# Optimization experiments

Measured on AMD Instinct MI355X. Metric: run time of the kernel, lower is better.

Reference implementation:

```python
import jax, jax.numpy as jnp
import numpy as np

NUM_GROUPS = 8
EPS = 1e-5


def setup_inputs() -> dict:
    key = jax.random.key(0)
    ks = jax.random.split(key, 4)
    C = 128
    x = jax.random.normal(ks[0], (4, C, 64, 64), dtype=jnp.float32)
    gn_weight = jnp.ones((C,), dtype=jnp.float32)
    gn_bias = jnp.zeros((C,), dtype=jnp.float32)
    qkv_weight = jax.random.normal(ks[1], (3 * C, C), dtype=jnp.float32) * (C ** -0.5)
    qkv_bias = jnp.zeros((3 * C,), dtype=jnp.float32)
    proj_weight = jax.random.normal(ks[2], (C, C), dtype=jnp.float32) * (C ** -0.5)
    proj_bias = jnp.zeros((C,), dtype=jnp.float32)
    return {
        "x": x,
        "gn_weight": gn_weight,
        "gn_bias": gn_bias,
        "qkv_weight": qkv_weight,
        "qkv_bias": qkv_bias,
        "proj_weight": proj_weight,
        "proj_bias": proj_bias,
    }


def reference(x, gn_weight, gn_bias, qkv_weight, qkv_bias, proj_weight, proj_bias):
    b, c, h, w = x.shape
    scale = c ** (-0.5)

    # GroupNorm(8, c): normalize over (channels_in_group, h, w)
    xg = x.reshape(b, NUM_GROUPS, c // NUM_GROUPS, h, w)
    mean = jnp.mean(xg, axis=(2, 3, 4), keepdims=True)
    var = jnp.var(xg, axis=(2, 3, 4), keepdims=True)
    xn = ((xg - mean) * jax.lax.rsqrt(var + EPS)).reshape(b, c, h, w)
    xn = xn * gn_weight[None, :, None, None] + gn_bias[None, :, None, None]

    # 1x1 conv QKV == channel matmul; flatten spatial to sequence n = h*w
    xn_flat = xn.reshape(b, c, h * w)  # [b, c, n]
    qkv = jnp.einsum('oc,bcn->bno', qkv_weight, xn_flat) + qkv_bias  # [b, n, 3c]
    q, k, v = qkv[..., :c], qkv[..., c:2 * c], qkv[..., 2 * c:]

    # attention: materializes [b, n, n] scores as in original
    attn = jnp.einsum('bnc,bmc->bnm', q, k) * scale
    attn = jax.nn.softmax(attn, axis=-1)
    out = jnp.einsum('bnm,bmc->bnc', attn, v)  # [b, n, c]

    # proj 1x1 conv + residual
    out = jnp.einsum('oc,bnc->bno', proj_weight, out) + proj_bias  # [b, n, c]
    out = out.transpose(0, 2, 1).reshape(b, c, h, w)
    return x + out
```

## Files before the change

### kernel.cpp

```cpp
#include <hip/hip_runtime.h>

#define BATCH 4
#define CCH 128
#define NSP 4096
#define NGRP 8
#define GROUP_ELEMS 65536
#define QSCALE 0.12751744f
#define EPS_GN 1e-5f
#define KHN 4
#define OPSTRIDE 2097152
#define LPSTRIDE 16384

typedef short s8b __attribute__((ext_vector_type(8)));
typedef float f32x4 __attribute__((ext_vector_type(4)));
typedef float f32x16 __attribute__((ext_vector_type(16)));

static __device__ __forceinline__ short f2bf(float f) {
  union { float f; unsigned u; } v; v.f = f;
  unsigned r = (v.u + 0x7FFFu + ((v.u >> 16) & 1u)) >> 16;
  return (short)r;
}

static __device__ __forceinline__ float bf2f(short s) {
  unsigned u = ((unsigned)(unsigned short)s) << 16;
  float f; __builtin_memcpy(&f, &u, 4); return f;
}

static __device__ __forceinline__ float fexp2(float x) {
#if __has_builtin(__builtin_amdgcn_exp2f)
  return __builtin_amdgcn_exp2f(x);
#else
  return exp2f(x);
#endif
}

static __device__ __forceinline__ unsigned cvtpk(float a, float b) {
  unsigned r;
  asm("v_cvt_pk_bf16_f32 %0, %1, %2" : "=v"(r) : "v"(a), "v"(b));
  return r;
}

static __device__ __forceinline__ s8b pack8(float a0, float a1, float a2, float a3,
                                            float a4, float a5, float a6, float a7) {
  union { unsigned u[4]; s8b v; } x;
  x.u[0] = cvtpk(a0, a1); x.u[1] = cvtpk(a2, a3);
  x.u[2] = cvtpk(a4, a5); x.u[3] = cvtpk(a6, a7);
  return x.v;
}

static __device__ __forceinline__ f32x4 mfma16(s8b a, s8b b, f32x4 c) {
  return __builtin_amdgcn_mfma_f32_16x16x32_bf16(a, b, c, 0, 0, 0);
}
static __device__ __forceinline__ f32x16 mfma32(s8b a, s8b b, f32x16 c) {
  return __builtin_amdgcn_mfma_f32_32x32x16_bf16(a, b, c, 0, 0, 0);
}

static __device__ __forceinline__ void async16(const void* g, void* l) {
  __builtin_amdgcn_global_load_lds(
      (const __attribute__((address_space(1))) void*)g,
      (__attribute__((address_space(3))) void*)l, 16, 0, 0);
}

__global__ void gn_stats(const float* __restrict__ x, float* __restrict__ part) {
  int bx = blockIdx.x;
  int ch = bx & 7, bg = bx >> 3;
  const float* base = x + (size_t)bg * GROUP_ELEMS + (size_t)ch * 8192;
  int t = threadIdx.x;
  float s = 0.f, ss = 0.f;
  #pragma unroll
  for (int i = 0; i < 8; ++i) {
    float4 v = *(const float4*)(base + i * 1024 + t * 4);
    s  += v.x + v.y + v.z + v.w;
    ss += v.x * v.x + v.y * v.y + v.z * v.z + v.w * v.w;
  }
  #pragma unroll
  for (int off = 1; off < 64; off <<= 1) {
    s  += __shfl_xor(s, off);
    ss += __shfl_xor(ss, off);
  }
  __shared__ float red[8];
  int w = t >> 6;
  if ((t & 63) == 0) { red[w * 2] = s; red[w * 2 + 1] = ss; }
  __syncthreads();
  if (t == 0) {
    part[bx * 2]     = red[0] + red[2] + red[4] + red[6];
    part[bx * 2 + 1] = red[1] + red[3] + red[5] + red[7];
  }
}

__global__ void gn_apply(const float* __restrict__ x, const float* __restrict__ gw,
                         const float* __restrict__ gb, const float* __restrict__ part,
                         short* __restrict__ xn) {
  int bx = blockIdx.x;
  int ns = bx & 7, g = (bx >> 3) & 7, b = bx >> 6;
  int bg = b * NGRP + g;
  float s = 0.f, ss = 0.f;
  #pragma unroll
  for (int j = 0; j < 8; ++j) {
    s  += part[(bg * 8 + j) * 2];
    ss += part[(bg * 8 + j) * 2 + 1];
  }
  float mean = s * (1.f / GROUP_ELEMS);
  float var  = ss * (1.f / GROUP_ELEMS) - mean * mean;
  float inv  = rsqrtf(var + EPS_GN);
  int t = threadIdx.x;
  int cl = t & 15, n4 = t >> 4;
  int c = g * 16 + cl;
  float ga = gw[c] * inv;
  float be = gb[c] - mean * ga;
  const float* xr = x + (size_t)(b * CCH + c) * NSP;
  short* xo = xn + (size_t)b * NSP * CCH + c;
  #pragma unroll
  for (int i = 0; i < 8; ++i) {
    int n = ns * 512 + i * 64 + n4 * 4;
    float4 v = *(const float4*)(xr + n);
    xo[(size_t)(n + 0) * CCH] = f2bf(v.x * ga + be);
    xo[(size_t)(n + 1) * CCH] = f2bf(v.y * ga + be);
    xo[(size_t)(n + 2) * CCH] = f2bf(v.z * ga + be);
    xo[(size_t)(n + 3) * CCH] = f2bf(v.w * ga + be);
  }
}

__global__ void qkv_gemm(const short* __restrict__ xn, const float* __restrict__ Wqkv,
                         const float* __restrict__ bias, short* __restrict__ q,
                         short* __restrict__ k, short* __restrict__ vt) {
  __shared__ short Xl[128 * 136];
  __shared__ short Wl[64 * 136];
  int bx = blockIdx.x;
  int t = threadIdx.x;
  int lane = t & 63, w = t >> 6, l15 = lane & 15, quad = lane >> 4;
  if (bx < 1024) {
    int ot = bx & 3, nt = (bx >> 2) & 63, b = bx >> 8;
    for (int idx = t; idx < 64 * 16; idx += 256) {
      int row = idx >> 4, c8 = idx & 15;
      *(s8b*)&Xl[row * 136 + c8 * 8] =
          *(const s8b*)(xn + ((size_t)(b * NSP + nt * 64 + row)) * CCH + c8 * 8);
    }
    for (int idx = t; idx < 64 * 16; idx += 256) {
      int row = idx >> 4, c8 = idx & 15;
      const float* src = Wqkv + (size_t)(ot * 64 + row) * CCH + c8 * 8;
      s8b wv;
      #pragma unroll
      for (int j = 0; j < 8; ++j) wv[j] = f2bf(src[j]);
      *(s8b*)&Wl[row * 136 + c8 * 8] = wv;
    }
    __syncthreads();
    s8b a[4];
    #pragma unroll
    for (int kc = 0; kc < 4; ++kc)
      a[kc] = *(const s8b*)&Xl[(w * 16 + l15) * 136 + kc * 32 + quad * 8];
    #pragma unroll
    for (int o4 = 0; o4 < 4; ++o4) {
      f32x4 acc = {0.f, 0.f, 0.f, 0.f};
      #pragma unroll
      for (int kc = 0; kc < 4; ++kc) {
        s8b bw = *(const s8b*)&Wl[(o4 * 16 + l15) * 136 + kc * 32 + quad * 8];
        acc = mfma16(a[kc], bw, acc);
      }
      int obase = ot * 64 + o4 * 16;
      short* dst = (obase < 128) ? q : k;
      float mulf = (obase < 128) ? QSCALE : 1.0f;
      int oc = obase - ((obase < 128) ? 0 : 128) + l15;
      float bs = bias[obase + l15];
      #pragma unroll
      for (int r = 0; r < 4; ++r) {
        int n = nt * 64 + w * 16 + quad * 4 + r;
        dst[((size_t)(b * NSP + n)) * CCH + oc] = f2bf((acc[r] + bs) * mulf);
      }
    }
  } else {
    int vbx = bx - 1024;
    int ot = vbx & 1, nt = (vbx >> 1) & 31, b = vbx >> 6;
    for (int idx = t; idx < 128 * 16; idx += 256) {
      int row = idx >> 4, c8 = idx & 15;
      *(s8b*)&Xl[row * 136 + c8 * 8] =
          *(const s8b*)(xn + ((size_t)(b * NSP + nt * 128 + row)) * CCH + c8 * 8);
    }
    for (int idx = t; idx < 64 * 16; idx += 256) {
      int row = idx >> 4, c8 = idx & 15;
      const float* src = Wqkv + (size_t)(256 + ot * 64 + row) * CCH + c8 * 8;
      s8b wv;
      #pragma unroll
      for (int j = 0; j < 8; ++j) wv[j] = f2bf(src[j]);
      *(s8b*)&Wl[row * 136 + c8 * 8] = wv;
    }
    __syncthreads();
    s8b a[4];
    #pragma unroll
    for (int kc = 0; kc < 4; ++kc)
      a[kc] = *(const s8b*)&Wl[(w * 16 + l15) * 136 + kc * 32 + quad * 8];
    float bs[4];
    #pragma unroll
    for (int r = 0; r < 4; ++r) bs[r] = bias[256 + ot * 64 + w * 16 + quad * 4 + r];
    int ppos = 8 * ((l15 >> 2) & 1) + (l15 & 3) + 4 * (l15 >> 3);
    #pragma unroll
    for (int ntile = 0; ntile < 8; ++ntile) {
      f32x4 acc = {0.f, 0.f, 0.f, 0.f};
      #pragma unroll
      for (int kc = 0; kc < 4; ++kc) {
        s8b bx2 = *(const s8b*)&Xl[(ntile * 16 + l15) * 136 + kc * 32 + quad * 8];
        acc = mfma16(a[kc], bx2, acc);
      }
      int npos = nt * 128 + ntile * 16 + ppos;
      #pragma unroll
      for (int r = 0; r < 4; ++r) {
        int og = ot * 64 + w * 16 + quad * 4 + r;
        vt[((size_t)(b * CCH + og)) * NSP + npos] = f2bf(acc[r] + bs[r]);
      }
    }
  }
}

__global__ __launch_bounds__(256, 2) void flash(const short* __restrict__ q,
                                                const short* __restrict__ k,
                                                const short* __restrict__ vt,
                                                short* __restrict__ Op,
                                                float* __restrict__ Lp) {
  int bx = blockIdx.x;
  int kh = bx & 3, b = (bx >> 2) & 3, qt = bx >> 4;
  __shared__ short Kl[2][64 * 128];
  __shared__ short Vl[2][128 * 64];
  int t = threadIdx.x;
  int lane = t & 63, w = t >> 6;
  int l31 = lane & 31, h = lane >> 5;
  int x15 = l31 & 15, x7 = l31 & 7;
  const short* kbase = k + (size_t)b * NSP * CCH;
  const short* vbase = vt + (size_t)b * CCH * NSP;
  int kt0 = kh * 1024;

  int krow_in_chunk = lane >> 4, kgrp = lane & 15;
  int vrow_in_chunk = lane >> 3, vgrp = lane & 7;

  s8b aq[8];
  {
    const short* qp = q + ((size_t)(b * NSP + qt * 128 + w * 32 + l31)) * CCH + h * 8;
    #pragma unroll
    for (int kc = 0; kc < 8; ++kc) aq[kc] = *(const s8b*)(qp + kc * 16);
  }
  f32x16 O[4];
  #pragma unroll
  for (int cg = 0; cg < 4; ++cg)
    #pragma unroll
    for (int r = 0; r < 16; ++r) O[cg][r] = 0.f;
  float lsum = 0.f;

  #define STAGE(buf_, key0_)                                                        \
    {                                                                               \
      const int key0v = (key0_);                                                    \
      _Pragma("unroll") for (int si = 0; si < 4; ++si) {                            \
        int c = w * 4 + si;                                                         \
        int rt = c * 4 + krow_in_chunk;                                             \
        async16(kbase + (size_t)(key0v + rt) * CCH + ((kgrp ^ (rt & 15)) * 8),      \
                &Kl[buf_][c * 512]);                                                \
        int rc = c * 8 + vrow_in_chunk;                                             \
        async16(vbase + (size_t)rc * NSP + key0v + ((vgrp ^ (rc & 7)) * 8),         \
                &Vl[buf_][c * 512]);                                                \
      }                                                                             \
    }

  STAGE(0, kt0)
  STAGE(1, kt0 + 64)

  for (int i = 0; i < 16; ++i) {
    int buf = i & 1;
    if (i < 15) {
      asm volatile("s_waitcnt vmcnt(8)\n\ts_barrier" ::: "memory");
    } else {
      asm volatile("s_waitcnt vmcnt(0)\n\ts_barrier" ::: "memory");
    }

    f32x16 st0, st1;
    #pragma unroll
    for (int r = 0; r < 16; ++r) { st0[r] = 0.f; st1[r] = 0.f; }
    const short* kp0 = &Kl[buf][(l31) * 128];
    const short* kp1 = &Kl[buf][(32 + l31) * 128];
    __builtin_amdgcn_s_setprio(1);
    #pragma unroll
    for (int kc = 0; kc < 8; ++kc) {
      int go = ((kc * 2 + h) ^ x15) * 8;
      s8b ak0 = *(const s8b*)&kp0[go];
      s8b ak1 = *(const s8b*)&kp1[go];
      st0 = mfma32(ak0, aq[kc], st0);
      st1 = mfma32(ak1, aq[kc], st1);
    }
    __builtin_amdgcn_s_setprio(0);

    s8b pb[4];
    {
      float pp[16];
      #pragma unroll
      for (int r = 0; r < 16; ++r) pp[r] = fexp2(st0[r]);
      lsum += (((pp[0] + pp[1]) + (pp[2] + pp[3])) + ((pp[4] + pp[5]) + (pp[6] + pp[7]))) +
              (((pp[8] + pp[9]) + (pp[10] + pp[11])) + ((pp[12] + pp[13]) + (pp[14] + pp[15])));
      pb[0] = pack8(pp[0], pp[1], pp[2], pp[3], pp[4], pp[5], pp[6], pp[7]);
      pb[1] = pack8(pp[8], pp[9], pp[10], pp[11], pp[12], pp[13], pp[14], pp[15]);
    }
    {
      float pp[16];
      #pragma unroll
      for (int r = 0; r < 16; ++r) pp[r] = fexp2(st1[r]);
      lsum += (((pp[0] + pp[1]) + (pp[2] + pp[3])) + ((pp[4] + pp[5]) + (pp[6] + pp[7]))) +
              (((pp[8] + pp[9]) + (pp[10] + pp[11])) + ((pp[12] + pp[13]) + (pp[14] + pp[15])));
      pb[2] = pack8(pp[0], pp[1], pp[2], pp[3], pp[4], pp[5], pp[6], pp[7]);
      pb[3] = pack8(pp[8], pp[9], pp[10], pp[11], pp[12], pp[13], pp[14], pp[15]);
    }

    __builtin_amdgcn_s_setprio(1);
    #pragma unroll
    for (int cg = 0; cg < 4; ++cg) {
      const short* vp = &Vl[buf][(cg * 32 + l31) * 64];
      #pragma unroll
      for (int kc2 = 0; kc2 < 4; ++kc2) {
        s8b av = *(const s8b*)&vp[((kc2 * 2 + h) ^ x7) * 8];
        O[cg] = mfma32(av, pb[kc2], O[cg]);
      }
    }
    __builtin_amdgcn_s_setprio(0);

    asm volatile("s_waitcnt lgkmcnt(0)\n\ts_barrier" ::: "memory");
    if (i < 14) STAGE(buf, kt0 + (i + 2) * 64)
  }

  lsum += __shfl_xor(lsum, 32);

  short* eb = &Kl[0][0] + w * 4096;
  #pragma unroll
  for (int cg = 0; cg < 4; ++cg)
    #pragma unroll
    for (int rp = 0; rp < 8; ++rp) {
      int r = rp * 2;
      int chlo = (r & 3) + 4 * h;
      int chhi = cg * 4 + (r >> 2);
      *(unsigned*)&eb[l31 * 128 + ((chhi ^ x7)) * 8 + chlo] = cvtpk(O[cg][r], O[cg][r + 1]);
    }
  short* ob = Op + (size_t)kh * OPSTRIDE + ((size_t)(b * NSP + qt * 128)) * CCH;
  float* lp = Lp + kh * LPSTRIDE + b * NSP + qt * 128;
  if (lane < 32) lp[w * 32 + l31] = lsum;
  __syncthreads();
  for (int idx = t; idx < 128 * 16; idx += 256) {
    int row = idx >> 4, c8 = idx & 15;
    int w2 = row >> 5, nl = row & 31;
    *(s8b*)(ob + (size_t)row * CCH + c8 * 8) =
        *(const s8b*)(&Kl[0][0] + w2 * 4096 + nl * 128 + ((c8 ^ (nl & 7))) * 8);
  }
}

__global__ void proj_gemm(const short* __restrict__ Op, const float* __restrict__ Lp,
                          const float* __restrict__ Wp, const float* __restrict__ pbias,
                          const float* __restrict__ x, float* __restrict__ out) {
  int bx = blockIdx.x;
  int nt = bx & 63, b = bx >> 6;
  __shared__ short Wl[128][136];
  int t = threadIdx.x;
  for (int idx = t; idx < 128 * 16; idx += 256) {
    int row = idx >> 4, c8 = idx & 15;
    const float* src = Wp + (size_t)row * CCH + c8 * 8;
    s8b wv;
    #pragma unroll
    for (int j = 0; j < 8; ++j) wv[j] = f2bf(src[j]);
    *(s8b*)&Wl[row][c8 * 8] = wv;
  }
  __syncthreads();
  int lane = t & 63, w = t >> 6, l15 = lane & 15, quad = lane >> 4;
  int row = nt * 64 + w * 16 + l15;
  float lsum = 0.f;
  #pragma unroll
  for (int s = 0; s < KHN; ++s) lsum += Lp[(size_t)s * LPSTRIDE + b * NSP + row];
  float linv = 1.f / lsum;
  const short* ap = Op + ((size_t)(b * NSP + row)) * CCH + quad * 8;
  s8b bfr[4];
  #pragma unroll
  for (int kc = 0; kc < 4; ++kc) {
    float acc8[8];
    #pragma unroll
    for (int j = 0; j < 8; ++j) acc8[j] = 0.f;
    #pragma unroll
    for (int s = 0; s < KHN; ++s) {
      s8b tv = *(const s8b*)(ap + (size_t)s * OPSTRIDE + kc * 32);
      #pragma unroll
      for (int j = 0; j < 8; ++j) acc8[j] += bf2f(tv[j]);
    }
    #pragma unroll
    for (int j = 0; j < 8; ++j) bfr[kc][j] = f2bf(acc8[j] * linv);
  }
  #pragma unroll
  for (int cg = 0; cg < 8; ++cg) {
    f32x4 acc = {0.f, 0.f, 0.f, 0.f};
    #pragma unroll
    for (int kc = 0; kc < 4; ++kc) {
      s8b aw = *(const s8b*)&Wl[cg * 16 + l15][kc * 32 + quad * 8];
      acc = mfma16(aw, bfr[kc], acc);
    }
    #pragma unroll
    for (int r = 0; r < 4; ++r) {
      int co = cg * 16 + quad * 4 + r;
      int n = nt * 64 + w * 16 + l15;
      size_t off = ((size_t)(b * CCH + co)) * NSP + n;
      out[off] = x[off] + acc[r] + pbias[co];
    }
  }
}

extern "C" void kernel_launch(void* const* d_in, const int* in_sizes, int n_in,
                              void* d_out, int out_size, void* d_ws, size_t ws_size,
                              hipStream_t stream) {
  (void)in_sizes; (void)n_in; (void)out_size; (void)ws_size;
  const float* x    = (const float*)d_in[0];
  const float* gw   = (const float*)d_in[1];
  const float* gb   = (const float*)d_in[2];
  const float* Wqkv = (const float*)d_in[3];
  const float* bqkv = (const float*)d_in[4];
  const float* Wp   = (const float*)d_in[5];
  const float* bp   = (const float*)d_in[6];
  float* out = (float*)d_out;
  char* ws = (char*)d_ws;
  float* part = (float*)ws;
  short* xn    = (short*)(ws + 4096);
  short* q     = (short*)(ws + 4096 + 1ull * 4194304);
  short* k     = (short*)(ws + 4096 + 2ull * 4194304);
  short* vt    = (short*)(ws + 4096 + 3ull * 4194304);
  short* Opart = (short*)(ws + 4096 + 4ull * 4194304);
  float* Lpart = (float*)(ws + 4096 + 8ull * 4194304);

  gn_stats<<<256, 256, 0, stream>>>(x, part);
  gn_apply<<<256, 256, 0, stream>>>(x, gw, gb, part, xn);
  qkv_gemm<<<1280, 256, 0, stream>>>(xn, Wqkv, bqkv, q, k, vt);
  flash<<<512, 256, 0, stream>>>(q, k, vt, Opart, Lpart);
  proj_gemm<<<256, 256, 0, stream>>>(Opart, Lpart, Wp, bp, x, out);
}
```

Measured before the change: 134.0 us.

## Pre-convert weights to bf16 once in gn_stats and widen QKV GEMM tiles

```diff
diff --git a/kernel.cpp b/kernel.cpp
--- a/kernel.cpp
+++ b/kernel.cpp
@@ -10,6 +10,8 @@
 #define KHN 4
 #define OPSTRIDE 2097152
 #define LPSTRIDE 16384
+#define WQKV_ELEMS 49152
+#define WP_ELEMS 16384
 
 typedef short s8b __attribute__((ext_vector_type(8)));
 typedef float f32x4 __attribute__((ext_vector_type(4)));
@@ -61,11 +63,18 @@
       (__attribute__((address_space(3))) void*)l, 16, 0, 0);
 }
 
-__global__ void gn_stats(const float* __restrict__ x, float* __restrict__ part) {
+__global__ void gn_stats(const float* __restrict__ x, float* __restrict__ part,
+                         const float* __restrict__ Wq, const float* __restrict__ Wpf,
+                         short* __restrict__ wbf) {
   int bx = blockIdx.x;
+  int t = threadIdx.x;
+  {
+    int base = bx * 256 + t;
+    float v = (base < WQKV_ELEMS) ? Wq[base] : Wpf[base - WQKV_ELEMS];
+    wbf[base] = f2bf(v);
+  }
   int ch = bx & 7, bg = bx >> 3;
   const float* base = x + (size_t)bg * GROUP_ELEMS + (size_t)ch * 8192;
-  int t = threadIdx.x;
   float s = 0.f, ss = 0.f;
   #pragma unroll
   for (int i = 0; i < 8; ++i) {
@@ -121,43 +130,34 @@
   }
 }
 
-__global__ void qkv_gemm(const short* __restrict__ xn, const float* __restrict__ Wqkv,
+__global__ void qkv_gemm(const short* __restrict__ xn, const short* __restrict__ wbf,
                          const float* __restrict__ bias, short* __restrict__ q,
                          short* __restrict__ k, short* __restrict__ vt) {
   __shared__ short Xl[128 * 136];
-  __shared__ short Wl[64 * 136];
   int bx = blockIdx.x;
   int t = threadIdx.x;
   int lane = t & 63, w = t >> 6, l15 = lane & 15, quad = lane >> 4;
-  if (bx < 1024) {
-    int ot = bx & 3, nt = (bx >> 2) & 63, b = bx >> 8;
+  if (bx < 256) {
+    int nt = bx & 63, b = bx >> 6;
     for (int idx = t; idx < 64 * 16; idx += 256) {
       int row = idx >> 4, c8 = idx & 15;
       *(s8b*)&Xl[row * 136 + c8 * 8] =
           *(const s8b*)(xn + ((size_t)(b * NSP + nt * 64 + row)) * CCH + c8 * 8);
     }
-    for (int idx = t; idx < 64 * 16; idx += 256) {
-      int row = idx >> 4, c8 = idx & 15;
-      const float* src = Wqkv + (size_t)(ot * 64 + row) * CCH + c8 * 8;
-      s8b wv;
-      #pragma unroll
-      for (int j = 0; j < 8; ++j) wv[j] = f2bf(src[j]);
-      *(s8b*)&Wl[row * 136 + c8 * 8] = wv;
-    }
     __syncthreads();
     s8b a[4];
     #pragma unroll
     for (int kc = 0; kc < 4; ++kc)
       a[kc] = *(const s8b*)&Xl[(w * 16 + l15) * 136 + kc * 32 + quad * 8];
     #pragma unroll
-    for (int o4 = 0; o4 < 4; ++o4) {
+    for (int og = 0; og < 16; ++og) {
       f32x4 acc = {0.f, 0.f, 0.f, 0.f};
       #pragma unroll
       for (int kc = 0; kc < 4; ++kc) {
-        s8b bw = *(const s8b*)&Wl[(o4 * 16 + l15) * 136 + kc * 32 + quad * 8];
+        s8b bw = *(const s8b*)(wbf + (size_t)(og * 16 + l15) * CCH + kc * 32 + quad * 8);
         acc = mfma16(a[kc], bw, acc);
       }
-      int obase = ot * 64 + o4 * 16;
+      int obase = og * 16;
       short* dst = (obase < 128) ? q : k;
       float mulf = (obase < 128) ? QSCALE : 1.0f;
       int oc = obase - ((obase < 128) ? 0 : 128) + l15;
@@ -169,43 +169,44 @@
       }
     }
   } else {
-    int vbx = bx - 1024;
-    int ot = vbx & 1, nt = (vbx >> 1) & 31, b = vbx >> 6;
+    int vbx = bx - 256;
+    int nt = vbx & 31, b = vbx >> 5;
     for (int idx = t; idx < 128 * 16; idx += 256) {
       int row = idx >> 4, c8 = idx & 15;
       *(s8b*)&Xl[row * 136 + c8 * 8] =
           *(const s8b*)(xn + ((size_t)(b * NSP + nt * 128 + row)) * CCH + c8 * 8);
     }
-    for (int idx = t; idx < 64 * 16; idx += 256) {
-      int row = idx >> 4, c8 = idx & 15;
-      const float* src = Wqkv + (size_t)(256 + ot * 64 + row) * CCH + c8 * 8;
-      s8b wv;
-      #pragma unroll
-      for (int j = 0; j < 8; ++j) wv[j] = f2bf(src[j]);
-      *(s8b*)&Wl[row * 136 + c8 * 8] = wv;
-    }
     __syncthreads();
-    s8b a[4];
-    #pragma unroll
-    for (int kc = 0; kc < 4; ++kc)
-      a[kc] = *(const s8b*)&Wl[(w * 16 + l15) * 136 + kc * 32 + quad * 8];
-    float bs[4];
-    #pragma unroll
-    for (int r = 0; r < 4; ++r) bs[r] = bias[256 + ot * 64 + w * 16 + quad * 4 + r];
+    const short* Wv = wbf + 256 * CCH;
+    s8b a0[4], a1[4];
+    #pragma unroll
+    for (int kc = 0; kc < 4; ++kc) {
+      a0[kc] = *(const s8b*)(Wv + (size_t)(w * 16 + l15) * CCH + kc * 32 + quad * 8);
+      a1[kc] = *(const s8b*)(Wv + (size_t)(64 + w * 16 + l15) * CCH + kc * 32 + quad * 8);
+    }
+    float bs0[4], bs1[4];
+    #pragma unroll
+    for (int r = 0; r < 4; ++r) {
+      bs0[r] = bias[256 + w * 16 + quad * 4 + r];
+      bs1[r] = bias[256 + 64 + w * 16 + quad * 4 + r];
+    }
     int ppos = 8 * ((l15 >> 2) & 1) + (l15 & 3) + 4 * (l15 >> 3);
     #pragma unroll
     for (int ntile = 0; ntile < 8; ++ntile) {
-      f32x4 acc = {0.f, 0.f, 0.f, 0.f};
+      f32x4 acc0 = {0.f, 0.f, 0.f, 0.f};
+      f32x4 acc1 = {0.f, 0.f, 0.f, 0.f};
       #pragma unroll
       for (int kc = 0; kc < 4; ++kc) {
         s8b bx2 = *(const s8b*)&Xl[(ntile * 16 + l15) * 136 + kc * 32 + quad * 8];
-        acc = mfma16(a[kc], bx2, acc);
+        acc0 = mfma16(a0[kc], bx2, acc0);
+        acc1 = mfma16(a1[kc], bx2, acc1);
       }
       int npos = nt * 128 + ntile * 16 + ppos;
       #pragma unroll
       for (int r = 0; r < 4; ++r) {
-        int og = ot * 64 + w * 16 + quad * 4 + r;
-        vt[((size_t)(b * CCH + og)) * NSP + npos] = f2bf(acc[r] + bs[r]);
+        int og0 = w * 16 + quad * 4 + r;
+        vt[((size_t)(b * CCH + og0)) * NSP + npos] = f2bf(acc0[r] + bs0[r]);
+        vt[((size_t)(b * CCH + 64 + og0)) * NSP + npos] = f2bf(acc1[r] + bs1[r]);
       }
     }
   }
@@ -346,21 +347,11 @@
 }
 
 __global__ void proj_gemm(const short* __restrict__ Op, const float* __restrict__ Lp,
-                          const float* __restrict__ Wp, const float* __restrict__ pbias,
+                          const short* __restrict__ wpbf, const float* __restrict__ pbias,
                           const float* __restrict__ x, float* __restrict__ out) {
   int bx = blockIdx.x;
   int nt = bx & 63, b = bx >> 6;
-  __shared__ short Wl[128][136];
   int t = threadIdx.x;
-  for (int idx = t; idx < 128 * 16; idx += 256) {
-    int row = idx >> 4, c8 = idx & 15;
-    const float* src = Wp + (size_t)row * CCH + c8 * 8;
-    s8b wv;
-    #pragma unroll
-    for (int j = 0; j < 8; ++j) wv[j] = f2bf(src[j]);
-    *(s8b*)&Wl[row][c8 * 8] = wv;
-  }
-  __syncthreads();
   int lane = t & 63, w = t >> 6, l15 = lane & 15, quad = lane >> 4;
   int row = nt * 64 + w * 16 + l15;
   float lsum = 0.f;
@@ -388,7 +379,7 @@
     f32x4 acc = {0.f, 0.f, 0.f, 0.f};
     #pragma unroll
     for (int kc = 0; kc < 4; ++kc) {
-      s8b aw = *(const s8b*)&Wl[cg * 16 + l15][kc * 32 + quad * 8];
+      s8b aw = *(const s8b*)(wpbf + (size_t)(cg * 16 + l15) * CCH + kc * 32 + quad * 8);
       acc = mfma16(aw, bfr[kc], acc);
     }
     #pragma unroll
@@ -421,10 +412,11 @@
   short* vt    = (short*)(ws + 4096 + 3ull * 4194304);
   short* Opart = (short*)(ws + 4096 + 4ull * 4194304);
   float* Lpart = (float*)(ws + 4096 + 8ull * 4194304);
-
-  gn_stats<<<256, 256, 0, stream>>>(x, part);
+  short* wbf   = (short*)(ws + 4096 + 8ull * 4194304 + 262144);
+
+  gn_stats<<<256, 256, 0, stream>>>(x, part, Wqkv, Wp, wbf);
   gn_apply<<<256, 256, 0, stream>>>(x, gw, gb, part, xn);
-  qkv_gemm<<<1280, 256, 0, stream>>>(xn, Wqkv, bqkv, q, k, vt);
+  qkv_gemm<<<384, 256, 0, stream>>>(xn, wbf, bqkv, q, k, vt);
   flash<<<512, 256, 0, stream>>>(q, k, vt, Opart, Lpart);
-  proj_gemm<<<256, 256, 0, stream>>>(Opart, Lpart, Wp, bp, x, out);
-}
+  proj_gemm<<<256, 256, 0, stream>>>(Opart, Lpart, wbf + WQKV_ELEMS, bp, x, out);
+}
```

Result: slower. 145.3 us (+8.4%).
